# Kernel tuning notes

Hardware: AMD Instinct MI355X
Metric: run time of the kernel (lower is better)

The kernel has to match this reference:

```python
import jax, jax.numpy as jnp
import numpy as np

NUM_HEADS = 4
EPS = 1e-12  # torch F.normalize eps


def conv1x1(x, w):
    # x: (b,c,h,w), w: (co,ci,1,1) -> pointwise conv == channel GEMM
    return jnp.einsum('bchw,dc->bdhw', x, w[:, :, 0, 0])


def dwconv3x3(x, w):
    # depthwise 3x3, groups = channels; w: (c,1,3,3)
    c = x.shape[1]
    return jax.lax.conv_general_dilated(
        x, w, window_strides=(1, 1), padding=((1, 1), (1, 1)),
        dimension_numbers=('NCHW', 'OIHW', 'NCHW'), feature_group_count=c)


def l2_normalize(x, axis=-1):
    n = jnp.sqrt(jnp.sum(x * x, axis=axis, keepdims=True))
    return x / jnp.maximum(n, EPS)


def setup_inputs() -> dict:
    key = jax.random.key(0)
    ks = jax.random.split(key, 8)
    b, c, h, w = 4, 192, 128, 128
    s = 0.05
    return {
        'x': jax.random.normal(ks[0], (b, c, h, w), jnp.float32),
        'wq': jax.random.normal(ks[1], (c, c, 1, 1), jnp.float32) * s,
        'wq_dw': jax.random.normal(ks[2], (c, 1, 3, 3), jnp.float32) * s,
        'wk': jax.random.normal(ks[3], (c, c, 1, 1), jnp.float32) * s,
        'wk_dw': jax.random.normal(ks[4], (c, 1, 3, 3), jnp.float32) * s,
        'wv': jax.random.normal(ks[5], (c, c, 1, 1), jnp.float32) * s,
        'wv_dw': jax.random.normal(ks[6], (c, 1, 3, 3), jnp.float32) * s,
        'temperature': jnp.ones((NUM_HEADS, 1, 1), jnp.float32),
    }


def reference(x, wq, wq_dw, wk, wk_dw, wv, wv_dw, temperature):
    b, c, h, w = x.shape
    hd = NUM_HEADS
    ch = c // hd  # per-head channels
    n = h * w

    q = dwconv3x3(conv1x1(x, wq), wq_dw)
    k = dwconv3x3(conv1x1(x, wk), wk_dw)
    v = dwconv3x3(conv1x1(x, wv), wv_dw)

    # b (head c) h w -> b head c (h w)
    q = q.reshape(b, hd, ch, n)
    k = k.reshape(b, hd, ch, n)
    v = v.reshape(b, hd, ch, n)

    q = l2_normalize(q, axis=-1)
    k = l2_normalize(k, axis=-1)

    # channel-wise attention: (c x N) @ (N x c) -> (c x c)
    attn = jnp.einsum('bhcn,bhdn->bhcd', q, k) * temperature  # temperature: (head,1,1)
    attn = jax.nn.softmax(attn, axis=-1)
    out = jnp.einsum('bhcd,bhdn->bhcn', attn, v)
    return out.reshape(b, c, h, w)
```

## Files before the change

### kernel.cpp

```cpp
#include <hip/hip_runtime.h>
#include <hip/hip_bf16.h>


typedef __attribute__((ext_vector_type(8))) short short8;
typedef __attribute__((ext_vector_type(4))) float f32x4;

#define NB 4
#define NC 192
#define NN 16384
#define CH 48
#define NWELEM 115780
#define NZERO 38400

__device__ inline unsigned short f2bf(float f) {
  union { float f; unsigned int u; } c; c.f = f;
  unsigned int r = c.u + 0x7FFF + ((c.u >> 16) & 1);
  return (unsigned short)(r >> 16);
}
__device__ inline float bf2f(unsigned short u) {
  union { unsigned int u; float f; } c; c.u = ((unsigned int)u) << 16;
  return c.f;
}

__device__ inline bool detect_f32(const unsigned short* x) {
  int l = threadIdx.x & 63;
  unsigned short u = x[2 * (l * 997 + 1)];
  int e = (u >> 7) & 0xFF;
  bool extreme = (e < 90) || (e > 165);
  return __popcll(__ballot(extreme)) >= 8;
}

__global__ __launch_bounds__(256) void k_pre(const unsigned short* __restrict__ x,
                                             const void* wq, const void* wk, const void* wv,
                                             const void* wqd, const void* wkd, const void* wvd,
                                             const void* temp,
                                             unsigned short* __restrict__ canon,
                                             float* __restrict__ zbase) {
  int blk = blockIdx.x;
  if (blk >= 453) {
    int i = (blk - 453) * 256 + threadIdx.x;
    if (i < NZERO) zbase[i] = 0.f;
    return;
  }
  bool f32 = detect_f32(x);
  int i = blk * 256 + threadIdx.x;
  if (i >= NWELEM) return;
  const void* src; int off;
  if (i < 36864)       { src = wq;  off = i; }
  else if (i < 73728)  { src = wk;  off = i - 36864; }
  else if (i < 110592) { src = wv;  off = i - 73728; }
  else if (i < 112320) { src = wqd; off = i - 110592; }
  else if (i < 114048) { src = wkd; off = i - 112320; }
  else if (i < 115776) { src = wvd; off = i - 114048; }
  else                 { src = temp; off = i - 115776; }
  canon[i] = f32 ? f2bf(((const float*)src)[off])
                 : ((const unsigned short*)src)[off];
}

__global__ __launch_bounds__(256) void k_transpose(const unsigned short* __restrict__ X,
                                                   unsigned short* __restrict__ Xt) {
  __shared__ unsigned short tile[64 * 65];
  bool f32 = detect_f32(X);
  int b = blockIdx.z, c0 = blockIdx.y * 64, p0 = blockIdx.x * 64;
  int tid = threadIdx.x;
  if (f32) {
    const float* Xf = (const float*)X;
    for (int it = 0; it < 16; ++it) {
      int idx = it * 256 + tid;
      int c = idx >> 6, p = idx & 63;
      tile[c * 65 + p] = f2bf(Xf[((size_t)b * NC + c0 + c) * NN + p0 + p]);
    }
  } else {
    for (int it = 0; it < 16; ++it) {
      int idx = it * 256 + tid;
      int c = idx >> 6, p = idx & 63;
      tile[c * 65 + p] = X[((size_t)b * NC + c0 + c) * NN + p0 + p];
    }
  }
  __syncthreads();
  for (int it = 0; it < 2; ++it) {
    int idx = it * 256 + tid;
    int cc = idx & 7, p = idx >> 3;
    short8 v;
#pragma unroll
    for (int j = 0; j < 8; ++j) v[j] = (short)tile[(cc * 8 + j) * 65 + p];
    *(short8*)(Xt + ((size_t)b * NN + p0 + p) * NC + c0 + cc * 8) = v;
  }
}

#define LDP 200
__global__ __launch_bounds__(256) void k_conv(const unsigned short* __restrict__ Wall,
                                              const unsigned short* __restrict__ Xt,
                                              unsigned short* __restrict__ Yall) {
  __shared__ __align__(16) unsigned short Xs[128 * LDP];
  int b = blockIdx.y, p0 = blockIdx.x * 128;
  int tid = threadIdx.x;
  const unsigned short* tb = Xt + ((size_t)b * NN + p0) * NC;
  for (int it = 0; it < 12; ++it) {
    int idx = it * 256 + tid;
    short8 v = *(const short8*)(tb + idx * 8);
    int p = idx / 24, cc = idx % 24;
    *(short8*)(&Xs[p * LDP + cc * 8]) = v;
  }
  __syncthreads();
  int lane = tid & 63, w = tid >> 6;
  int wm = w & 1, wn = w >> 1;
  int lrow = lane & 15, lq = lane >> 4;
  short8 bf[6][4];
  for (int ks = 0; ks < 6; ++ks)
    for (int nt = 0; nt < 4; ++nt)
      bf[ks][nt] = *(const short8*)(&Xs[(wn * 64 + nt * 16 + lrow) * LDP + ks * 32 + lq * 8]);
  for (int dt = 0; dt < 9; ++dt) {
    int d0 = dt * 64;
    f32x4 acc[2][4];
    for (int mt = 0; mt < 2; ++mt)
      for (int nt = 0; nt < 4; ++nt) acc[mt][nt] = (f32x4){0.f, 0.f, 0.f, 0.f};
    for (int ks = 0; ks < 6; ++ks) {
      int k = ks * 32 + lq * 8;
      short8 a[2];
      for (int mt = 0; mt < 2; ++mt)
        a[mt] = *(const short8*)(Wall + (size_t)(d0 + wm * 32 + mt * 16 + lrow) * NC + k);
      for (int mt = 0; mt < 2; ++mt)
        for (int nt = 0; nt < 4; ++nt)
          acc[mt][nt] = __builtin_amdgcn_mfma_f32_16x16x32_bf16(a[mt], bf[ks][nt], acc[mt][nt], 0, 0, 0);
    }
    int proj = dt / 3, c0 = (dt % 3) * 64;
    unsigned short* Yb = Yall + (((size_t)proj * NB + b) * NC) * NN;
    for (int mt = 0; mt < 2; ++mt)
      for (int nt = 0; nt < 4; ++nt)
        for (int r = 0; r < 4; ++r) {
          int c = c0 + wm * 32 + mt * 16 + lq * 4 + r;
          int p = p0 + wn * 64 + nt * 16 + lrow;
          Yb[(size_t)c * NN + p] = f2bf(acc[mt][nt][r]);
        }
  }
}

__device__ inline void cvtrow(short8 raw, unsigned short lo, unsigned short hi,
                              float* dst) {
  dst[0] = bf2f(lo);
#pragma unroll
  for (int j = 0; j < 8; ++j) dst[j + 1] = bf2f((unsigned short)raw[j]);
  dst[9] = bf2f(hi);
}

__global__ __launch_bounds__(256) void k_dwconv(const unsigned short* __restrict__ Yall,
                                                const unsigned short* __restrict__ Wdall,
                                                unsigned short* __restrict__ Pq,
                                                unsigned short* __restrict__ Pk,
                                                unsigned short* __restrict__ Pv,
                                                float* __restrict__ ssq,
                                                float* __restrict__ ssk) {
  int y = blockIdx.x, b = blockIdx.y;
  int proj = y / NC, c = y % NC;
  int tid = threadIdx.x;
  int lane = tid & 63, ch = tid & 15, rg = tid >> 4;
  const unsigned short* base = Yall + (((size_t)proj * NB + b) * NC + c) * NN;
  unsigned short* P = (proj == 0 ? Pq : (proj == 1 ? Pk : Pv));
  float* ss = (proj == 0 ? ssq : (proj == 1 ? ssk : nullptr));
  int r0 = rg * 8;

  short8 raw[10];
  unsigned short hl[10], hr[10];
#pragma unroll
  for (int i = 0; i < 10; ++i) {
    int gy = r0 - 1 + i;
    const unsigned short* rp = base + gy * 128 + ch * 8;
    if (gy >= 0 && gy < 128) {
      raw[i] = *(const short8*)rp;
      hl[i] = (ch > 0)  ? rp[-1] : (unsigned short)0;
      hr[i] = (ch < 15) ? rp[8]  : (unsigned short)0;
    } else {
      raw[i] = (short8){0, 0, 0, 0, 0, 0, 0, 0};
      hl[i] = 0;
      hr[i] = 0;
    }
  }

  float wk9[9];
#pragma unroll
  for (int i = 0; i < 9; ++i) wk9[i] = bf2f(Wdall[(proj * NC + c) * 9 + i]);

  float rows[3][10];
  cvtrow(raw[0], hl[0], hr[0], rows[0]);
  cvtrow(raw[1], hl[1], hr[1], rows[1]);
  float ssacc = 0.f;
#pragma unroll
  for (int r = 0; r < 8; ++r) {
    cvtrow(raw[r + 2], hl[r + 2], hr[r + 2], rows[(r + 2) % 3]);
    float z[8];
#pragma unroll
    for (int j = 0; j < 8; ++j) z[j] = 0.f;
#pragma unroll
    for (int dy = 0; dy < 3; ++dy) {
      const float* f = rows[(r + dy) % 3];
      float w0 = wk9[dy * 3], w1 = wk9[dy * 3 + 1], w2 = wk9[dy * 3 + 2];
#pragma unroll
      for (int j = 0; j < 8; ++j) z[j] += w0 * f[j] + w1 * f[j + 1] + w2 * f[j + 2];
    }
    short8 sv;
#pragma unroll
    for (int j = 0; j < 8; ++j) { sv[j] = (short)f2bf(z[j]); ssacc += z[j] * z[j]; }
    *(short8*)(P + ((size_t)b * NC + c) * NN + (r0 + r) * 128 + ch * 8) = sv;
  }
  if (ss) {
    for (int off = 32; off; off >>= 1) ssacc += __shfl_down(ssacc, off);
    if (lane == 0) atomicAdd(&ss[b * NC + c], ssacc);
  }
}

__global__ __launch_bounds__(256) void k_attn(const unsigned short* __restrict__ Qp,
                                              const unsigned short* __restrict__ Kp,
                                              float* __restrict__ S) {
  __shared__ float Sred[CH * CH];
  int bh = blockIdx.y, chunk = blockIdx.x;
  int b = bh >> 2, h = bh & 3;
  int tid = threadIdx.x, lane = tid & 63, w = tid >> 6;
  int lrow = lane & 15, lq = lane >> 4;
  const unsigned short* Qb = Qp + ((size_t)b * NC + h * CH) * NN;
  const unsigned short* Kb = Kp + ((size_t)b * NC + h * CH) * NN;
  int nbase = chunk * 1024 + w * 256;
  f32x4 acc[3][3];
  for (int i = 0; i < 3; ++i)
    for (int j = 0; j < 3; ++j) acc[i][j] = (f32x4){0.f, 0.f, 0.f, 0.f};
  for (int ks = 0; ks < 8; ++ks) {
    int n = nbase + ks * 32 + lq * 8;
    short8 a[3], bb[3];
    for (int t = 0; t < 3; ++t) a[t]  = *(const short8*)(Qb + (size_t)(t * 16 + lrow) * NN + n);
    for (int t = 0; t < 3; ++t) bb[t] = *(const short8*)(Kb + (size_t)(t * 16 + lrow) * NN + n);
    for (int ti = 0; ti < 3; ++ti)
      for (int tj = 0; tj < 3; ++tj)
        acc[ti][tj] = __builtin_amdgcn_mfma_f32_16x16x32_bf16(a[ti], bb[tj], acc[ti][tj], 0, 0, 0);
  }
  for (int i = tid; i < CH * CH; i += 256) Sred[i] = 0.f;
  __syncthreads();
  for (int ti = 0; ti < 3; ++ti)
    for (int tj = 0; tj < 3; ++tj)
      for (int r = 0; r < 4; ++r) {
        int row = ti * 16 + lq * 4 + r, col = tj * 16 + lrow;
        atomicAdd(&Sred[row * CH + col], acc[ti][tj][r]);
      }
  __syncthreads();
  float* Sg = S + bh * (CH * CH);
  for (int i = tid; i < CH * CH; i += 256) atomicAdd(&Sg[i], Sred[i]);
}

__global__ void k_softmax(const float* __restrict__ S, const float* __restrict__ ssq,
                          const float* __restrict__ ssk, const unsigned short* __restrict__ tempc,
                          float* __restrict__ AT) {
  int bh = blockIdx.x, b = bh >> 2, h = bh & 3;
  int i = threadIdx.x;
  if (i >= CH) return;
  float t = bf2f(tempc[h]);
  float rq = 1.f / fmaxf(sqrtf(ssq[b * NC + h * CH + i]), 1e-12f);
  const float* Srow = S + bh * (CH * CH) + i * CH;
  float l[CH];
  float m = -1e30f;
  for (int j = 0; j < CH; ++j) {
    float rk = 1.f / fmaxf(sqrtf(ssk[b * NC + h * CH + j]), 1e-12f);
    l[j] = Srow[j] * rq * rk * t;
    m = fmaxf(m, l[j]);
  }
  float s = 0.f;
  for (int j = 0; j < CH; ++j) { l[j] = __expf(l[j] - m); s += l[j]; }
  float inv = 1.f / s;
  for (int j = 0; j < CH; ++j) AT[bh * (CH * CH) + j * CH + i] = l[j] * inv;
}

__global__ __launch_bounds__(256) void k_out(const float* __restrict__ AT,
                                             const unsigned short* __restrict__ Vp,
                                             void* __restrict__ Out,
                                             const unsigned short* __restrict__ x) {
  bool f32 = detect_f32(x);
  int bh = blockIdx.y, b = bh >> 2, h = bh & 3;
  int p0 = (blockIdx.x * 256 + threadIdx.x) * 2;
  const float* A = AT + bh * (CH * CH);
  const unsigned short* Vb = Vp + ((size_t)b * NC + h * CH) * NN;
  float a1[CH], a2[CH];
  for (int i = 0; i < CH; ++i) { a1[i] = 0.f; a2[i] = 0.f; }
  for (int j = 0; j < CH; ++j) {
    unsigned int u = *(const unsigned int*)(Vb + (size_t)j * NN + p0);
    float v1 = bf2f((unsigned short)(u & 0xFFFF));
    float v2 = bf2f((unsigned short)(u >> 16));
    const float* Aj = A + j * CH;
    for (int i = 0; i < CH; ++i) {
      float a = Aj[i];
      a1[i] += a * v1;
      a2[i] += a * v2;
    }
  }
  size_t obase = ((size_t)b * NC + h * CH) * NN;
  if (f32) {
    float* Of = (float*)Out;
    for (int i = 0; i < CH; ++i)
      *(float2*)(Of + obase + (size_t)i * NN + p0) = make_float2(a1[i], a2[i]);
  } else {
    unsigned short* Ob = (unsigned short*)Out;
    for (int i = 0; i < CH; ++i) {
      unsigned int u = ((unsigned int)f2bf(a2[i]) << 16) | f2bf(a1[i]);
      *(unsigned int*)(Ob + obase + (size_t)i * NN + p0) = u;
    }
  }
}

extern "C" void kernel_launch(void* const* d_in, const int* in_sizes, int n_in,
                              void* d_out, int out_size, void* d_ws, size_t ws_size,
                              hipStream_t stream) {
  const unsigned short* x = (const unsigned short*)d_in[0];

  const size_t TEN = (size_t)NB * NC * NN;
  unsigned short* bufA = (unsigned short*)d_ws;
  unsigned short* bufB = bufA + TEN;
  unsigned short* bufV = bufB + TEN;
  unsigned short* Xt   = bufV + TEN;
  unsigned short* Yall = Xt + TEN;
  float* ssq = (float*)(Yall + 3 * TEN);
  float* ssk = ssq + NB * NC;
  float* S   = ssk + NB * NC;
  float* AT  = S + 16 * CH * CH;
  unsigned short* canon = (unsigned short*)(AT + 16 * CH * CH);
  const unsigned short* Wall = canon;
  const unsigned short* Wdall = canon + 110592;
  const unsigned short* Tmp = canon + 115776;

  k_pre<<<453 + (NZERO + 255) / 256, 256, 0, stream>>>(
      x, d_in[1], d_in[3], d_in[5], d_in[2], d_in[4], d_in[6], d_in[7], canon, ssq);
  k_transpose<<<dim3(NN / 64, NC / 64, NB), 256, 0, stream>>>(x, Xt);
  k_conv<<<dim3(NN / 128, NB), 256, 0, stream>>>(Wall, Xt, Yall);
  k_dwconv<<<dim3(3 * NC, NB), 256, 0, stream>>>(Yall, Wdall, bufA, bufB, bufV, ssq, ssk);
  k_attn<<<dim3(16, 16), 256, 0, stream>>>(bufA, bufB, S);
  k_softmax<<<16, 64, 0, stream>>>(S, ssq, ssk, Tmp, AT);
  k_out<<<dim3(NN / 512, 16), 256, 0, stream>>>(AT, bufV, d_out, x);
}
```

Measured before the change: 244.7 us.

## Fuse input transpose into pointwise conv by loading MFMA fragments directly from NCHW

Removes the separate transpose kernel and its bf16 Xt workspace round trip. The pointwise-conv GEMM now builds its B fragments straight from the channel-major input, converting fp32 to bf16 in registers. This saves a launch and a full tensor write/read. In exchange, each fragment needs eight strided loads one channel plane apart, with no LDS staging. Adjacent lanes still read adjacent pixels, so accesses stay partly coalesced.

```diff
diff --git a/kernel.cpp b/kernel.cpp
--- a/kernel.cpp
+++ b/kernel.cpp
@@ -57,59 +57,42 @@
                  : ((const unsigned short*)src)[off];
 }
 
-__global__ __launch_bounds__(256) void k_transpose(const unsigned short* __restrict__ X,
-                                                   unsigned short* __restrict__ Xt) {
-  __shared__ unsigned short tile[64 * 65];
+__global__ __launch_bounds__(256) void k_conv(const unsigned short* __restrict__ Wall,
+                                              const unsigned short* __restrict__ X,
+                                              unsigned short* __restrict__ Yall) {
   bool f32 = detect_f32(X);
-  int b = blockIdx.z, c0 = blockIdx.y * 64, p0 = blockIdx.x * 64;
-  int tid = threadIdx.x;
-  if (f32) {
-    const float* Xf = (const float*)X;
-    for (int it = 0; it < 16; ++it) {
-      int idx = it * 256 + tid;
-      int c = idx >> 6, p = idx & 63;
-      tile[c * 65 + p] = f2bf(Xf[((size_t)b * NC + c0 + c) * NN + p0 + p]);
-    }
-  } else {
-    for (int it = 0; it < 16; ++it) {
-      int idx = it * 256 + tid;
-      int c = idx >> 6, p = idx & 63;
-      tile[c * 65 + p] = X[((size_t)b * NC + c0 + c) * NN + p0 + p];
-    }
-  }
-  __syncthreads();
-  for (int it = 0; it < 2; ++it) {
-    int idx = it * 256 + tid;
-    int cc = idx & 7, p = idx >> 3;
-    short8 v;
-#pragma unroll
-    for (int j = 0; j < 8; ++j) v[j] = (short)tile[(cc * 8 + j) * 65 + p];
-    *(short8*)(Xt + ((size_t)b * NN + p0 + p) * NC + c0 + cc * 8) = v;
-  }
-}
-
-#define LDP 200
-__global__ __launch_bounds__(256) void k_conv(const unsigned short* __restrict__ Wall,
-                                              const unsigned short* __restrict__ Xt,
-                                              unsigned short* __restrict__ Yall) {
-  __shared__ __align__(16) unsigned short Xs[128 * LDP];
   int b = blockIdx.y, p0 = blockIdx.x * 128;
   int tid = threadIdx.x;
-  const unsigned short* tb = Xt + ((size_t)b * NN + p0) * NC;
-  for (int it = 0; it < 12; ++it) {
-    int idx = it * 256 + tid;
-    short8 v = *(const short8*)(tb + idx * 8);
-    int p = idx / 24, cc = idx % 24;
-    *(short8*)(&Xs[p * LDP + cc * 8]) = v;
-  }
-  __syncthreads();
   int lane = tid & 63, w = tid >> 6;
   int wm = w & 1, wn = w >> 1;
   int lrow = lane & 15, lq = lane >> 4;
   short8 bf[6][4];
-  for (int ks = 0; ks < 6; ++ks)
-    for (int nt = 0; nt < 4; ++nt)
-      bf[ks][nt] = *(const short8*)(&Xs[(wn * 64 + nt * 16 + lrow) * LDP + ks * 32 + lq * 8]);
+  if (f32) {
+    const float* Xf = (const float*)X;
+#pragma unroll
+    for (int ks = 0; ks < 6; ++ks)
+#pragma unroll
+      for (int nt = 0; nt < 4; ++nt) {
+        int px = p0 + wn * 64 + nt * 16 + lrow;
+        const float* xp = Xf + ((size_t)b * NC + ks * 32 + lq * 8) * NN + px;
+        short8 v;
+#pragma unroll
+        for (int j = 0; j < 8; ++j) v[j] = (short)f2bf(xp[(size_t)j * NN]);
+        bf[ks][nt] = v;
+      }
+  } else {
+#pragma unroll
+    for (int ks = 0; ks < 6; ++ks)
+#pragma unroll
+      for (int nt = 0; nt < 4; ++nt) {
+        int px = p0 + wn * 64 + nt * 16 + lrow;
+        const unsigned short* xp = X + ((size_t)b * NC + ks * 32 + lq * 8) * NN + px;
+        short8 v;
+#pragma unroll
+        for (int j = 0; j < 8; ++j) v[j] = (short)xp[(size_t)j * NN];
+        bf[ks][nt] = v;
+      }
+  }
   for (int dt = 0; dt < 9; ++dt) {
     int d0 = dt * 64;
     f32x4 acc[2][4];
@@ -312,8 +295,7 @@
   unsigned short* bufA = (unsigned short*)d_ws;
   unsigned short* bufB = bufA + TEN;
   unsigned short* bufV = bufB + TEN;
-  unsigned short* Xt   = bufV + TEN;
-  unsigned short* Yall = Xt + TEN;
+  unsigned short* Yall = bufV + TEN;
   float* ssq = (float*)(Yall + 3 * TEN);
   float* ssk = ssq + NB * NC;
   float* S   = ssk + NB * NC;
@@ -325,8 +307,7 @@
 
   k_pre<<<453 + (NZERO + 255) / 256, 256, 0, stream>>>(
       x, d_in[1], d_in[3], d_in[5], d_in[2], d_in[4], d_in[6], d_in[7], canon, ssq);
-  k_transpose<<<dim3(NN / 64, NC / 64, NB), 256, 0, stream>>>(x, Xt);
-  k_conv<<<dim3(NN / 128, NB), 256, 0, stream>>>(Wall, Xt, Yall);
+  k_conv<<<dim3(NN / 128, NB), 256, 0, stream>>>(Wall, x, Yall);
   k_dwconv<<<dim3(3 * NC, NB), 256, 0, stream>>>(Yall, Wdall, bufA, bufB, bufV, ssq, ssk);
   k_attn<<<dim3(16, 16), 256, 0, stream>>>(bufA, bufB, S);
   k_softmax<<<16, 64, 0, stream>>>(S, ssq, ssk, Tmp, AT);
```

New measurement: 232.0 us. -5.2%, faster.
